# Optimization experiments

Measured on AMD Instinct MI355X. Metric: run time of the kernel, lower is better.

## Reference

```python
import math
import jax, jax.numpy as jnp
import numpy as np

B, P, S, E = 16, 128, 4096, 512
H = 8
D = E // H  # head dim = 64
LATENT = 128


def setup_inputs() -> dict:
    key = jax.random.key(0)
    ks = jax.random.split(key, 12)
    scale = 1.0 / math.sqrt(E)
    Q = jax.random.normal(ks[0], (B, P, E), dtype=jnp.float32)
    K = jax.random.normal(ks[1], (B, S, E), dtype=jnp.float32)
    V = jax.random.normal(ks[2], (B, S, E), dtype=jnp.float32)
    # boolean key-padding mask; guarantee at least one valid key per row
    mask = jax.random.uniform(ks[3], (B, S)) > 0.2
    mask = mask.at[:, 0].set(True)
    wq = jax.random.normal(ks[4], (E, E), dtype=jnp.float32) * scale
    bq = jnp.zeros((E,), dtype=jnp.float32)
    wk = jax.random.normal(ks[5], (E, E), dtype=jnp.float32) * scale
    bk = jnp.zeros((E,), dtype=jnp.float32)
    wv = jax.random.normal(ks[6], (E, E), dtype=jnp.float32) * scale
    bv = jnp.zeros((E,), dtype=jnp.float32)
    wo = jax.random.normal(ks[7], (E, LATENT), dtype=jnp.float32) * scale
    bo = jnp.zeros((LATENT,), dtype=jnp.float32)
    return {"Q": Q, "K": K, "V": V, "mask": mask,
            "wq": wq, "bq": bq, "wk": wk, "bk": bk,
            "wv": wv, "bv": bv, "wo": wo, "bo": bo}


def reference(Q, K, V, mask, wq, bq, wk, bk, wv, bv, wo, bo):
    b, p, e = Q.shape
    s = K.shape[1]
    # QKV projections, split into heads: (B, H, P/S, D)
    Qp = (Q @ wq + bq).reshape(b, p, H, D).transpose(0, 2, 1, 3)
    Kp = (K @ wk + bk).reshape(b, s, H, D).transpose(0, 2, 1, 3)
    Vp = (V @ wv + bv).reshape(b, s, H, D).transpose(0, 2, 1, 3)
    scores = jnp.einsum('bhpk,bhsk->bhps', Qp, Kp) / math.sqrt(D)
    # mask: (B,S) -> (B,1,1,S); masked_fill(~mask, -inf)
    neg_inf = jnp.finfo(scores.dtype).min
    scores = jnp.where(mask[:, None, None, :], scores, neg_inf)
    A = jax.nn.softmax(scores, axis=-1)
    C = jnp.einsum('bhps,bhsk->bhpk', A, Vp)
    C = C.transpose(0, 2, 1, 3).reshape(b, p, e)  # (B, P, E)
    return C @ wo + bo  # (B, P, LATENT)
```

## Files before the change

kernel.cpp:

```cpp
#include <hip/hip_runtime.h>
#include <hip/hip_bf16.h>
#include <stdint.h>


typedef _Float16 f16;
typedef __attribute__((ext_vector_type(4))) float f32x4;
typedef __attribute__((ext_vector_type(8))) _Float16 f16x8;
typedef __attribute__((ext_vector_type(4))) _Float16 f16x4;
typedef __attribute__((ext_vector_type(4))) float f4v;

__device__ __forceinline__ f32x4 mfma16(f16x8 a, f16x8 b, f32x4 c) {
    return __builtin_amdgcn_mfma_f32_16x16x32_f16(a, b, c, 0, 0, 0);
}
__device__ __forceinline__ void gload16(const void* g, void* l) {
    __builtin_amdgcn_global_load_lds(
        (const __attribute__((address_space(1))) void*)g,
        (__attribute__((address_space(3))) void*)l, 16, 0, 0);
}

__global__ __launch_bounds__(256) void mask_canon(const unsigned char* __restrict__ raw,
                                                  unsigned char* __restrict__ outb) {
    __shared__ int flags;
    const int tid = threadIdx.x;
    if (tid == 0) flags = 0;
    __syncthreads();
    unsigned w = ((const unsigned*)raw)[tid];
    int f = 0;
    if (w == 0x3F800000u) f = 2;
    else if (w & 0xFFFFFF00u) f = 1;
    if (f) atomicOr(&flags, f);
    __syncthreads();
    const int fl = flags;
    const bool asword = (fl & 2) || !(fl & 1);
    const int base = blockIdx.x * 1024;
    if (!asword) {
        ((unsigned*)(outb + base))[tid] = ((const unsigned*)(raw + base))[tid];
    } else {
        const unsigned* r32 = (const unsigned*)raw;
        const int e0 = base + tid * 4;
        unsigned o = 0;
#pragma unroll
        for (int j = 0; j < 4; j++) o |= (r32[e0 + j] ? 1u : 0u) << (8 * j);
        ((unsigned*)(outb + base))[tid] = o;
    }
}

__global__ void prep_w(const float* __restrict__ wq, const float* __restrict__ wk,
                       const float* __restrict__ wv,
                       f16* __restrict__ WqT, f16* __restrict__ WkT,
                       f16* __restrict__ WvT) {
    const int n = blockIdx.x;
    for (int k = threadIdx.x; k < 512; k += blockDim.x) {
        WqT[n * 512 + k] = (f16)wq[k * 512 + n];
        WkT[n * 512 + k] = (f16)wk[k * 512 + n];
        WvT[n * 512 + k] = (f16)wv[k * 512 + n];
    }
}

template <int VT, int QSC>
__global__ __launch_bounds__(256) void gemm_af32_bt(
    const float* __restrict__ A, const f16* __restrict__ Bt,
    const float* __restrict__ bias, f16* __restrict__ O) {
    __shared__ f16 lA[4096];
    __shared__ f16 lB[4096];
    const int tid = threadIdx.x, lane = tid & 63, wave = tid >> 6;
    const int p = blockIdx.x, nx = gridDim.x >> 3;
    const int L = (p & 7) * nx + (p >> 3);
    const int m0 = (L >> 2) * 128, n0 = (L & 3) * 128;
    const int wr = (wave >> 1) * 64, wc = (wave & 1) * 64;
    const int fr = lane & 15, fko = (lane >> 4) * 8;
    const int arow = wave * 32 + (lane >> 3);
    const int acol = (lane & 7) * 4;
    f32x4 acc[4][4] = {};
    for (int kk = 0; kk < 512; kk += 32) {
        __syncthreads();
        f4v x[4];
#pragma unroll
        for (int i = 0; i < 4; i++)
            x[i] = *(const f4v*)&A[(size_t)(m0 + arow + i * 8) * 512 + kk + acol];
#pragma unroll
        for (int i = 0; i < 2; i++) {
            const int ob = wave * 1024 + i * 4096;
            const int o = ob + (lane << 4);
            const int row = o >> 6, cb = o & 63;
            gload16((const char*)Bt + (size_t)(n0 + row) * 1024 + kk * 2 + cb,
                    (char*)lB + ob);
        }
#pragma unroll
        for (int i = 0; i < 4; i++) {
            f16x4 h4;
#pragma unroll
            for (int j = 0; j < 4; j++) h4[j] = (f16)x[i][j];
            *(f16x4*)&lA[(arow + i * 8) * 32 + acol] = h4;
        }
        __syncthreads();
        f16x8 ah[4];
#pragma unroll
        for (int m = 0; m < 4; m++)
            ah[m] = *(const f16x8*)&lA[(wr + m * 16 + fr) * 32 + fko];
#pragma unroll
        for (int n = 0; n < 4; n++) {
            f16x8 bh = *(const f16x8*)&lB[(wc + n * 16 + fr) * 32 + fko];
#pragma unroll
            for (int m = 0; m < 4; m++) acc[m][n] = mfma16(ah[m], bh, acc[m][n]);
        }
    }
#pragma unroll
    for (int mi = 0; mi < 4; mi++) {
#pragma unroll
        for (int ni = 0; ni < 4; ni++) {
            const int col = n0 + wc + ni * 16 + fr;
            const float bs = bias[col];
            if (VT) {
                const int gr0 = m0 + wr + mi * 16 + ((lane >> 4) << 2);
                const int b = gr0 >> 12, s = gr0 & 4095;
                const int h = col >> 6, d = col & 63;
                f16x4 pk;
#pragma unroll
                for (int r = 0; r < 4; r++) pk[r] = (f16)(acc[mi][ni][r] + bs);
                *(f16x4*)&O[((size_t)((b * 8 + h) * 64 + d)) * 4096 + s] = pk;
            } else {
#pragma unroll
                for (int r = 0; r < 4; r++) {
                    const int grow = m0 + wr + mi * 16 + ((lane >> 4) << 2) + r;
                    float v = acc[mi][ni][r] + bs;
                    if (QSC) v *= 0.125f;
                    O[(size_t)grow * 512 + col] = (f16)v;
                }
            }
        }
    }
}

__global__ __launch_bounds__(256) void attn_kern(
    const f16* __restrict__ Qp, const f16* __restrict__ Kp,
    const f16* __restrict__ VT, const unsigned char* __restrict__ mask,
    float* __restrict__ C) {
    __shared__ f16 lbuf[2][2 * 4096];
    __shared__ f16 lP[4 * 16 * 72];
    const int tid = threadIdx.x, lane = tid & 63, wave = tid >> 6;
    const int fr = lane & 15, fko = (lane >> 4) * 8;
    const int p_ = blockIdx.x;
    const int L = (p_ & 7) * 32 + (p_ >> 3);
    const int pblk = L & 1, h = (L >> 1) & 7, b = L >> 4;
    const int q0 = b * 128 + pblk * 64;
    const int qrow = q0 + wave * 16;

    f16x8 aq[2];
#pragma unroll
    for (int kp = 0; kp < 2; kp++)
        aq[kp] = *(const f16x8*)&Qp[(size_t)(qrow + fr) * 512 + h * 64 + kp * 32 + fko];
    f32x4 Ofr[4] = {};
    float lacc[4] = {0.f, 0.f, 0.f, 0.f};

    const size_t kbase = (size_t)b * 4096 * 512 + h * 64;
    const size_t vbase = (size_t)((b * 8 + h) * 64) * 4096;
    const unsigned char* mrow = mask + b * 4096;
    f16* lpw = &lP[wave * 1152];

    auto stage = [&](int c, int bi) {
        const int s0 = c * 64;
        char* dst = (char*)lbuf[bi];
#pragma unroll
        for (int i = 0; i < 2; i++) {
            const int ob = wave * 1024 + i * 4096;
            const int o = ob + (lane << 4);
            const int row = o >> 7, cb = o & 127;
            const int cbl = cb ^ ((row & 7) << 4);
            gload16((const char*)(Kp + kbase) + (size_t)(s0 + row) * 1024 + cbl,
                    dst + ob);
            gload16((const char*)VT + (vbase + (size_t)row * 4096 + s0) * 2 + cbl,
                    dst + 8192 + ob);
        }
    };

    stage(0, 0);
    __syncthreads();
    for (int c = 0; c < 64; c++) {
        const int cur = c & 1;
        if (c < 63) stage(c + 1, cur ^ 1);
        const f16* lK = lbuf[cur];
        const f16* lV = lK + 4096;
        const int s0 = c * 64;
        f32x4 sc[4];
#pragma unroll
        for (int nt = 0; nt < 4; nt++) {
            f32x4 s = {0.f, 0.f, 0.f, 0.f};
            const int kr = nt * 16 + fr;
            const int rb = kr * 128;
            const int sw = (kr & 7) << 4;
#pragma unroll
            for (int kp = 0; kp < 2; kp++) {
                const int cb = (kp * 32 + fko) * 2;
                f16x8 kb = *(const f16x8*)((const char*)lK + (rb + (cb ^ sw)));
                s = mfma16(aq[kp], kb, s);
            }
            if (!mrow[s0 + kr]) {
                f32x4 ninf = {-1e30f, -1e30f, -1e30f, -1e30f};
                s = ninf;
            }
            sc[nt] = s;
        }
#pragma unroll
        for (int nt = 0; nt < 4; nt++) {
#pragma unroll
            for (int r = 0; r < 4; r++) {
                const float pv = __expf(fminf(sc[nt][r], 11.0f));
                lacc[r] += pv;
                lpw[((lane >> 4) * 4 + r) * 72 + nt * 16 + fr] = (f16)pv;
            }
        }
        f16x8 pa[2];
#pragma unroll
        for (int kp = 0; kp < 2; kp++)
            pa[kp] = *(const f16x8*)&lpw[fr * 72 + kp * 32 + fko];
#pragma unroll
        for (int dt = 0; dt < 4; dt++) {
            const int vr = dt * 16 + fr;
            const int rb = vr * 128;
            const int sw = (vr & 7) << 4;
#pragma unroll
            for (int kp = 0; kp < 2; kp++) {
                const int cb = (kp * 32 + fko) * 2;
                f16x8 vb = *(const f16x8*)((const char*)lV + (rb + (cb ^ sw)));
                Ofr[dt] = mfma16(pa[kp], vb, Ofr[dt]);
            }
        }
        __syncthreads();
    }
    float l4[4];
#pragma unroll
    for (int r = 0; r < 4; r++) {
        float s = lacc[r];
#pragma unroll
        for (int d = 1; d < 16; d <<= 1) s += __shfl_xor(s, d);
        l4[r] = s;
    }
#pragma unroll
    for (int dt = 0; dt < 4; dt++)
#pragma unroll
        for (int r = 0; r < 4; r++) {
            const int q = qrow + (lane >> 4) * 4 + r;
            C[(size_t)q * 512 + h * 64 + dt * 16 + fr] = Ofr[dt][r] / l4[r];
        }
}

__global__ __launch_bounds__(128) void outproj(const float* __restrict__ C,
                                               const float* __restrict__ wo,
                                               const float* __restrict__ bo,
                                               float* __restrict__ out) {
    const int l = threadIdx.x;
    const int r0 = blockIdx.x * 8;
    float acc[8];
#pragma unroll
    for (int r = 0; r < 8; r++) acc[r] = 0.f;
#pragma unroll 4
    for (int e = 0; e < 512; e++) {
        const float w = wo[e * 128 + l];
#pragma unroll
        for (int r = 0; r < 8; r++) acc[r] = fmaf(C[(size_t)(r0 + r) * 512 + e], w, acc[r]);
    }
    const float bb = bo[l];
#pragma unroll
    for (int r = 0; r < 8; r++) out[(size_t)(r0 + r) * 128 + l] = acc[r] + bb;
}

extern "C" void kernel_launch(void* const* d_in, const int* in_sizes, int n_in,
                              void* d_out, int out_size, void* d_ws, size_t ws_size,
                              hipStream_t stream) {
    const float* Q = (const float*)d_in[0];
    const float* K = (const float*)d_in[1];
    const float* V = (const float*)d_in[2];
    const unsigned char* mraw = (const unsigned char*)d_in[3];
    const float* wq = (const float*)d_in[4];
    const float* bq = (const float*)d_in[5];
    const float* wk = (const float*)d_in[6];
    const float* bk = (const float*)d_in[7];
    const float* wv = (const float*)d_in[8];
    const float* bv = (const float*)d_in[9];
    const float* wo = (const float*)d_in[10];
    const float* bo = (const float*)d_in[11];
    (void)in_sizes; (void)n_in; (void)out_size; (void)ws_size;

    char* ws = (char*)d_ws;
    size_t off = 0;
    auto alloc = [&](size_t n) {
        char* p = ws + off;
        off = (off + n + 255) & ~(size_t)255;
        return p;
    };
    f16* WqT = (f16*)alloc(512 * 512 * 2);
    f16* WkT = (f16*)alloc(512 * 512 * 2);
    f16* WvT = (f16*)alloc(512 * 512 * 2);
    f16* Qp  = (f16*)alloc((size_t)2048 * 512 * 2);
    f16* Kp  = (f16*)alloc((size_t)65536 * 512 * 2);
    f16* VpT = (f16*)alloc((size_t)65536 * 512 * 2);
    float* C = (float*)alloc((size_t)2048 * 512 * 4);
    unsigned char* maskc = (unsigned char*)alloc(65536);

    mask_canon<<<64, 256, 0, stream>>>(mraw, maskc);
    prep_w<<<512, 256, 0, stream>>>(wq, wk, wv, WqT, WkT, WvT);
    gemm_af32_bt<0, 1><<<64, 256, 0, stream>>>(Q, WqT, bq, Qp);
    gemm_af32_bt<0, 0><<<2048, 256, 0, stream>>>(K, WkT, bk, Kp);
    gemm_af32_bt<1, 0><<<2048, 256, 0, stream>>>(V, WvT, bv, VpT);
    attn_kern<<<256, 256, 0, stream>>>(Qp, Kp, VpT, maskc, C);
    outproj<<<256, 128, 0, stream>>>(C, wo, bo, (float*)d_out);
}
```

Measured before the change: 586.5 us.

## Split attention over key chunks with combine kernel; swizzle GEMM LDS with K-step 64

Attention is split into four key-range partitions per query block, raising the grid from 256 to 1024 blocks. Each block writes unnormalized partial outputs and row sums, and a new combine kernel sums them and normalizes. The projection GEMM now stages 64-wide K slices with an XOR-swizzled LDS layout to halve barrier count and reduce bank conflicts. This costs extra global traffic for partial buffers and an additional kernel launch.

```diff
diff --git a/kernel.cpp b/kernel.cpp
--- a/kernel.cpp
+++ b/kernel.cpp
@@ -61,48 +61,70 @@
 __global__ __launch_bounds__(256) void gemm_af32_bt(
     const float* __restrict__ A, const f16* __restrict__ Bt,
     const float* __restrict__ bias, f16* __restrict__ O) {
-    __shared__ f16 lA[4096];
-    __shared__ f16 lB[4096];
+    __shared__ f16 lA[8192];
+    __shared__ f16 lB[8192];
     const int tid = threadIdx.x, lane = tid & 63, wave = tid >> 6;
     const int p = blockIdx.x, nx = gridDim.x >> 3;
     const int L = (p & 7) * nx + (p >> 3);
     const int m0 = (L >> 2) * 128, n0 = (L & 3) * 128;
     const int wr = (wave >> 1) * 64, wc = (wave & 1) * 64;
     const int fr = lane & 15, fko = (lane >> 4) * 8;
-    const int arow = wave * 32 + (lane >> 3);
-    const int acol = (lane & 7) * 4;
+    const int ar = wave * 32 + (lane >> 4);
+    const int ac = (lane & 15) * 4;
     f32x4 acc[4][4] = {};
-    for (int kk = 0; kk < 512; kk += 32) {
+    for (int kk = 0; kk < 512; kk += 64) {
         __syncthreads();
         f4v x[4];
 #pragma unroll
         for (int i = 0; i < 4; i++)
-            x[i] = *(const f4v*)&A[(size_t)(m0 + arow + i * 8) * 512 + kk + acol];
-#pragma unroll
-        for (int i = 0; i < 2; i++) {
-            const int ob = wave * 1024 + i * 4096;
-            const int o = ob + (lane << 4);
-            const int row = o >> 6, cb = o & 63;
-            gload16((const char*)Bt + (size_t)(n0 + row) * 1024 + kk * 2 + cb,
-                    (char*)lB + ob);
+            x[i] = *(const f4v*)&A[(size_t)(m0 + ar + i * 4) * 512 + kk + ac];
+#pragma unroll
+        for (int i = 0; i < 4; i++) {
+            const int o = wave * 4096 + i * 1024 + (lane << 4);
+            const int row = o >> 7, cb = o & 127;
+            const int cbl = cb ^ ((row & 7) << 4);
+            gload16((const char*)Bt + (size_t)(n0 + row) * 1024 + kk * 2 + cbl,
+                    (char*)lB + o);
         }
 #pragma unroll
         for (int i = 0; i < 4; i++) {
             f16x4 h4;
 #pragma unroll
             for (int j = 0; j < 4; j++) h4[j] = (f16)x[i][j];
-            *(f16x4*)&lA[(arow + i * 8) * 32 + acol] = h4;
+            const int row = ar + i * 4;
+            const int byte = (row * 128 + (lane & 15) * 8) ^ ((row & 7) << 4);
+            *(f16x4*)((char*)lA + byte) = h4;
+        }
+#pragma unroll
+        for (int i = 0; i < 4; i++)
+            x[i] = *(const f4v*)&A[(size_t)(m0 + ar + 16 + i * 4) * 512 + kk + ac];
+#pragma unroll
+        for (int i = 0; i < 4; i++) {
+            f16x4 h4;
+#pragma unroll
+            for (int j = 0; j < 4; j++) h4[j] = (f16)x[i][j];
+            const int row = ar + 16 + i * 4;
+            const int byte = (row * 128 + (lane & 15) * 8) ^ ((row & 7) << 4);
+            *(f16x4*)((char*)lA + byte) = h4;
         }
         __syncthreads();
-        f16x8 ah[4];
-#pragma unroll
-        for (int m = 0; m < 4; m++)
-            ah[m] = *(const f16x8*)&lA[(wr + m * 16 + fr) * 32 + fko];
-#pragma unroll
-        for (int n = 0; n < 4; n++) {
-            f16x8 bh = *(const f16x8*)&lB[(wc + n * 16 + fr) * 32 + fko];
-#pragma unroll
-            for (int m = 0; m < 4; m++) acc[m][n] = mfma16(ah[m], bh, acc[m][n]);
+#pragma unroll
+        for (int kp = 0; kp < 2; kp++) {
+            f16x8 ah[4];
+#pragma unroll
+            for (int m = 0; m < 4; m++) {
+                const int row = wr + m * 16 + fr;
+                const int byte = (row * 128 + kp * 64 + fko * 2) ^ ((row & 7) << 4);
+                ah[m] = *(const f16x8*)((const char*)lA + byte);
+            }
+#pragma unroll
+            for (int n = 0; n < 4; n++) {
+                const int row = wc + n * 16 + fr;
+                const int byte = (row * 128 + kp * 64 + fko * 2) ^ ((row & 7) << 4);
+                f16x8 bh = *(const f16x8*)((const char*)lB + byte);
+#pragma unroll
+                for (int m = 0; m < 4; m++) acc[m][n] = mfma16(ah[m], bh, acc[m][n]);
+            }
         }
     }
 #pragma unroll
@@ -135,16 +157,16 @@
 __global__ __launch_bounds__(256) void attn_kern(
     const f16* __restrict__ Qp, const f16* __restrict__ Kp,
     const f16* __restrict__ VT, const unsigned char* __restrict__ mask,
-    float* __restrict__ C) {
+    float* __restrict__ Cp, float* __restrict__ lp) {
     __shared__ f16 lbuf[2][2 * 4096];
     __shared__ f16 lP[4 * 16 * 72];
     const int tid = threadIdx.x, lane = tid & 63, wave = tid >> 6;
     const int fr = lane & 15, fko = (lane >> 4) * 8;
     const int p_ = blockIdx.x;
-    const int L = (p_ & 7) * 32 + (p_ >> 3);
-    const int pblk = L & 1, h = (L >> 1) & 7, b = L >> 4;
-    const int q0 = b * 128 + pblk * 64;
-    const int qrow = q0 + wave * 16;
+    const int L = (p_ & 7) * 128 + (p_ >> 3);
+    const int pblk = L & 1, split = (L >> 1) & 3, h = (L >> 3) & 7, b = L >> 6;
+    const int qrow = b * 128 + pblk * 64 + wave * 16;
+    const int sbase = split * 1024;
 
     f16x8 aq[2];
 #pragma unroll
@@ -159,7 +181,7 @@
     f16* lpw = &lP[wave * 1152];
 
     auto stage = [&](int c, int bi) {
-        const int s0 = c * 64;
+        const int s0 = sbase + c * 64;
         char* dst = (char*)lbuf[bi];
 #pragma unroll
         for (int i = 0; i < 2; i++) {
@@ -176,12 +198,12 @@
 
     stage(0, 0);
     __syncthreads();
-    for (int c = 0; c < 64; c++) {
+    for (int c = 0; c < 16; c++) {
         const int cur = c & 1;
-        if (c < 63) stage(c + 1, cur ^ 1);
+        if (c < 15) stage(c + 1, cur ^ 1);
         const f16* lK = lbuf[cur];
         const f16* lV = lK + 4096;
-        const int s0 = c * 64;
+        const int s0 = sbase + c * 64;
         f32x4 sc[4];
 #pragma unroll
         for (int nt = 0; nt < 4; nt++) {
@@ -236,13 +258,43 @@
         for (int d = 1; d < 16; d <<= 1) s += __shfl_xor(s, d);
         l4[r] = s;
     }
+    float* Cpo = Cp + (size_t)split * 2048 * 512;
 #pragma unroll
     for (int dt = 0; dt < 4; dt++)
 #pragma unroll
         for (int r = 0; r < 4; r++) {
             const int q = qrow + (lane >> 4) * 4 + r;
-            C[(size_t)q * 512 + h * 64 + dt * 16 + fr] = Ofr[dt][r] / l4[r];
-        }
+            Cpo[(size_t)q * 512 + h * 64 + dt * 16 + fr] = Ofr[dt][r];
+        }
+    if (fr == 0) {
+#pragma unroll
+        for (int r = 0; r < 4; r++) {
+            const int q = qrow + (lane >> 4) * 4 + r;
+            lp[split * 2048 * 8 + q * 8 + h] = l4[r];
+        }
+    }
+}
+
+__global__ __launch_bounds__(256) void combine(const float* __restrict__ Cp,
+                                               const float* __restrict__ lp,
+                                               float* __restrict__ C) {
+    const int q = blockIdx.x;
+    __shared__ float ls[8];
+    if (threadIdx.x < 8) {
+        float s = 0.f;
+#pragma unroll
+        for (int p = 0; p < 4; p++) s += lp[p * 2048 * 8 + q * 8 + threadIdx.x];
+        ls[threadIdx.x] = 1.0f / s;
+    }
+    __syncthreads();
+#pragma unroll
+    for (int j = 0; j < 2; j++) {
+        const int e = threadIdx.x + j * 256;
+        float c = 0.f;
+#pragma unroll
+        for (int p = 0; p < 4; p++) c += Cp[(size_t)p * 2048 * 512 + (size_t)q * 512 + e];
+        C[(size_t)q * 512 + e] = c * ls[e >> 6];
+    }
 }
 
 __global__ __launch_bounds__(128) void outproj(const float* __restrict__ C,
@@ -295,7 +347,9 @@
     f16* Qp  = (f16*)alloc((size_t)2048 * 512 * 2);
     f16* Kp  = (f16*)alloc((size_t)65536 * 512 * 2);
     f16* VpT = (f16*)alloc((size_t)65536 * 512 * 2);
-    float* C = (float*)alloc((size_t)2048 * 512 * 4);
+    float* Cp = (float*)alloc((size_t)4 * 2048 * 512 * 4);
+    float* lp = (float*)alloc((size_t)4 * 2048 * 8 * 4);
+    float* C  = (float*)alloc((size_t)2048 * 512 * 4);
     unsigned char* maskc = (unsigned char*)alloc(65536);
 
     mask_canon<<<64, 256, 0, stream>>>(mraw, maskc);
@@ -303,6 +357,7 @@
     gemm_af32_bt<0, 1><<<64, 256, 0, stream>>>(Q, WqT, bq, Qp);
     gemm_af32_bt<0, 0><<<2048, 256, 0, stream>>>(K, WkT, bk, Kp);
     gemm_af32_bt<1, 0><<<2048, 256, 0, stream>>>(V, WvT, bv, VpT);
-    attn_kern<<<256, 256, 0, stream>>>(Qp, Kp, VpT, maskc, C);
+    attn_kern<<<1024, 256, 0, stream>>>(Qp, Kp, VpT, maskc, Cp, lp);
+    combine<<<2048, 256, 0, stream>>>(Cp, lp, C);
     outproj<<<256, 128, 0, stream>>>(C, wo, bo, (float*)d_out);
 }
```

Result: faster. 529.3 us (-9.7%).
